# Kernel optimization log

Measured on AMD Instinct MI355X. Metric: run time of the kernel, lower is better.

The kernel has to match this reference:

```python
import jax, jax.numpy as jnp
import numpy as np

TEMPERATURE = 0.5
B, D = 4096, 256


def setup_inputs() -> dict:
    key = jax.random.key(0)
    k1, k2 = jax.random.split(key)
    emb_i = jax.random.normal(k1, (B, D), dtype=jnp.float32)
    emb_j = jax.random.normal(k2, (B, D), dtype=jnp.float32)
    return {"emb_i": emb_i, "emb_j": emb_j}


def reference(emb_i, emb_j):
    # NT-Xent (SimCLR) loss, vectorized version of the per-sample python loop.
    n = emb_i.shape[0]
    eps = 1e-12
    z_i = emb_i / jnp.maximum(jnp.linalg.norm(emb_i, axis=1, keepdims=True), eps)
    z_j = emb_j / jnp.maximum(jnp.linalg.norm(emb_j, axis=1, keepdims=True), eps)
    reps = jnp.concatenate([z_i, z_j], axis=0)               # [2N, D], unit rows
    # cosine similarity of unit vectors == dot product
    sim = reps @ reps.T                                       # [2N, 2N]
    exp_sim = jnp.exp(sim / TEMPERATURE)
    # denominator for row i: sum over k != i of exp(sim[i,k]/T)
    denom = jnp.sum(exp_sim, axis=1) - jnp.diagonal(exp_sim)  # [2N]
    # positive-pair sims: sim[k, k+N] and sim[k+N, k]
    pos = jnp.concatenate([jnp.diagonal(sim[:n, n:]), jnp.diagonal(sim[n:, :n])])
    # l_ij = log(exp(pos/T) / denom) = pos/T - log(denom)
    loss_terms = pos / TEMPERATURE - jnp.log(denom)
    return (1.0 / (2 * n)) * jnp.sum(loss_terms)
```

## Files before the change

kernel.cpp:

```cpp
#include <hip/hip_runtime.h>
#include <math.h>


#define NROWS 8192
#define NHALF 4096
#define DIM   256
#define BMT   256
#define NCB   (NROWS / 128)
#define NCBT  (NROWS / BMT)
#define NTRIT (NCBT * (NCBT + 1) / 2)

typedef __attribute__((ext_vector_type(8))) short bf16x8;
typedef __attribute__((ext_vector_type(4))) float f32x4;

static __device__ __forceinline__ unsigned short f2bf(float x) {
  unsigned int u = __float_as_uint(x);
  unsigned int r = (u + 0x7FFFu + ((u >> 16) & 1u)) >> 16;
  return (unsigned short)r;
}

__global__ __launch_bounds__(256) void normalize_kernel(
    const float* __restrict__ emb_i, const float* __restrict__ emb_j,
    unsigned short* __restrict__ zbF, float* __restrict__ out) {
  __shared__ unsigned short tile[16 * DIM];
  if (blockIdx.x == 0 && threadIdx.x == 0) out[0] = 0.f;
  const int w = threadIdx.x >> 6, lane = threadIdx.x & 63;
  const int rg = blockIdx.x;
  #pragma unroll
  for (int rr = 0; rr < 4; ++rr) {
    const int m16 = w * 4 + rr;
    const int row = rg * 16 + m16;
    const float* src = (row < NHALF) ? (emb_i + (size_t)row * DIM)
                                     : (emb_j + (size_t)(row - NHALF) * DIM);
    float4 v = ((const float4*)src)[lane];
    float ss = v.x * v.x + v.y * v.y + v.z * v.z + v.w * v.w;
    #pragma unroll
    for (int off = 32; off; off >>= 1) ss += __shfl_down(ss, off, 64);
    float total = __shfl(ss, 0, 64);
    float inv = 1.69870077f / fmaxf(sqrtf(total), 1e-12f);
    ushort4 o;
    o.x = f2bf(v.x * inv); o.y = f2bf(v.y * inv);
    o.z = f2bf(v.z * inv); o.w = f2bf(v.w * inv);
    const int s = lane >> 3, quad = (lane >> 1) & 3, jj = (lane & 1) * 4;
    *(ushort4*)&tile[s * 512 + (quad * 16 + m16) * 8 + jj] = o;
  }
  __syncthreads();
  uint4* dst = (uint4*)(zbF + (size_t)rg * (16 * DIM));
  const uint4* srcT = (const uint4*)tile;
  dst[threadIdx.x] = srcT[threadIdx.x];
  dst[256 + threadIdx.x] = srcT[256 + threadIdx.x];
}

__global__ __launch_bounds__(512, 2) void denom_kernel(
    const unsigned short* __restrict__ zbF, float* __restrict__ denomP,
    float* __restrict__ posv) {
  __shared__ unsigned short As[2][32 * 512];
  __shared__ unsigned short Bs[2][32 * 512];
  __shared__ float rowpart[4][256];
  __shared__ float colpart[2][256];

  int t = (blockIdx.x & 7) * (NTRIT / 8) + (blockIdx.x >> 3);
  int by = (int)((sqrtf(8.0f * (float)t + 1.0f) - 1.0f) * 0.5f);
  while ((by + 1) * (by + 2) / 2 <= t) ++by;
  while (by * (by + 1) / 2 > t) --by;
  int bx = t - by * (by + 1) / 2;

  const int tid = threadIdx.x;
  const int w = tid >> 6;
  const int lane = tid & 63;
  const int wr = w >> 2, wc = w & 3;
  const int quad = lane >> 4;
  const int m16 = lane & 15;
  const int row0 = bx * BMT;
  const int col0 = by * BMT;

  const unsigned short* gA = zbF + (size_t)(bx * 16) * 4096 + lane * 8;
  const unsigned short* gB = zbF + (size_t)(by * 16) * 4096 + lane * 8;

  f32x4 acc[8][4];
  #pragma unroll
  for (int i = 0; i < 8; ++i)
    #pragma unroll
    for (int j = 0; j < 4; ++j) {
      f32x4 z4 = {0.f, 0.f, 0.f, 0.f};
      acc[i][j] = z4;
    }

  auto stage = [&](int b, int kt) {
    #pragma unroll
    for (int cc = 0; cc < 4; ++cc) {
      const int c = w * 4 + cc;
      const size_t goff = (size_t)(c >> 1) * 4096 + (kt * 2 + (c & 1)) * 512;
      __builtin_amdgcn_global_load_lds(
          (const __attribute__((address_space(1))) unsigned int*)(gA + goff),
          (__attribute__((address_space(3))) unsigned int*)&As[b][c * 512],
          16, 0, 0);
      __builtin_amdgcn_global_load_lds(
          (const __attribute__((address_space(1))) unsigned int*)(gB + goff),
          (__attribute__((address_space(3))) unsigned int*)&Bs[b][c * 512],
          16, 0, 0);
    }
  };

  auto compute = [&](int b) {
    #pragma unroll
    for (int s32 = 0; s32 < 2; ++s32) {
      bf16x8 af[8], bf[4];
      #pragma unroll
      for (int i = 0; i < 8; ++i)
        af[i] = *(const bf16x8*)
            &As[b][((wr * 8 + i) * 2 + s32) * 512 + lane * 8];
      #pragma unroll
      for (int j = 0; j < 4; ++j)
        bf[j] = *(const bf16x8*)
            &Bs[b][((wc * 4 + j) * 2 + s32) * 512 + lane * 8];
      __builtin_amdgcn_s_setprio(1);
      #pragma unroll
      for (int i = 0; i < 8; ++i)
        #pragma unroll
        for (int j = 0; j < 4; ++j)
          acc[i][j] = __builtin_amdgcn_mfma_f32_16x16x32_bf16(
              af[i], bf[j], acc[i][j], 0, 0, 0);
      __builtin_amdgcn_s_setprio(0);
    }
  };

  stage(0, 0);
  stage(1, 1);
  asm volatile("s_waitcnt vmcnt(8)" ::: "memory");
  __builtin_amdgcn_s_barrier();
  asm volatile("" ::: "memory");
  compute(0);
  __builtin_amdgcn_s_barrier();
  asm volatile("" ::: "memory");
  stage(0, 2);
  asm volatile("s_waitcnt vmcnt(8)" ::: "memory");
  __builtin_amdgcn_s_barrier();
  asm volatile("" ::: "memory");
  compute(1);
  __builtin_amdgcn_s_barrier();
  asm volatile("" ::: "memory");
  stage(1, 3);
  asm volatile("s_waitcnt vmcnt(8)" ::: "memory");
  __builtin_amdgcn_s_barrier();
  asm volatile("" ::: "memory");
  compute(0);
  __builtin_amdgcn_s_barrier();
  asm volatile("" ::: "memory");
  asm volatile("s_waitcnt vmcnt(0)" ::: "memory");
  __builtin_amdgcn_s_barrier();
  asm volatile("" ::: "memory");
  compute(1);

  if (col0 - row0 == NHALF) {
    #pragma unroll
    for (int i = 0; i < 8; ++i)
      #pragma unroll
      for (int j = 0; j < 4; ++j) {
        int gcol = col0 + wc * 64 + j * 16 + m16;
        #pragma unroll
        for (int r = 0; r < 4; ++r) {
          int grow = row0 + wr * 128 + i * 16 + quad * 4 + r;
          if (gcol - grow == NHALF) posv[grow] = acc[i][j][r];
        }
      }
  }

  float rs[8][4];
  float cs[4] = {0.f, 0.f, 0.f, 0.f};
  #pragma unroll
  for (int i = 0; i < 8; ++i)
    #pragma unroll
    for (int r = 0; r < 4; ++r) rs[i][r] = 0.f;

  if (bx != by) {
    #pragma unroll
    for (int i = 0; i < 8; ++i)
      #pragma unroll
      for (int j = 0; j < 4; ++j)
        #pragma unroll
        for (int r = 0; r < 4; ++r) {
          float e = __builtin_amdgcn_exp2f(acc[i][j][r]);
          rs[i][r] += e;
          cs[j] += e;
        }
  } else {
    #pragma unroll
    for (int i = 0; i < 8; ++i)
      #pragma unroll
      for (int j = 0; j < 4; ++j) {
        int gcol = col0 + wc * 64 + j * 16 + m16;
        #pragma unroll
        for (int r = 0; r < 4; ++r) {
          int grow = row0 + wr * 128 + i * 16 + quad * 4 + r;
          float e =
              (grow == gcol) ? 0.f : __builtin_amdgcn_exp2f(acc[i][j][r]);
          rs[i][r] += e;
          cs[j] += e;
        }
      }
  }

  #pragma unroll
  for (int i = 0; i < 8; ++i)
    #pragma unroll
    for (int r = 0; r < 4; ++r) {
      float v = rs[i][r];
      v += __shfl_xor(v, 1, 16);
      v += __shfl_xor(v, 2, 16);
      v += __shfl_xor(v, 4, 16);
      v += __shfl_xor(v, 8, 16);
      if (m16 == 0) rowpart[wc][wr * 128 + i * 16 + quad * 4 + r] = v;
    }
  #pragma unroll
  for (int j = 0; j < 4; ++j) {
    float v = cs[j];
    v += __shfl_xor(v, 16, 64);
    v += __shfl_xor(v, 32, 64);
    if (quad == 0) colpart[wr][wc * 64 + j * 16 + m16] = v;
  }
  __syncthreads();

  if (tid < 256) {
    denomP[(size_t)(2 * by) * NROWS + row0 + tid] =
        rowpart[0][tid] + rowpart[1][tid] + rowpart[2][tid] + rowpart[3][tid];
  } else if (bx != by) {
    int c = tid - 256;
    denomP[(size_t)(2 * bx) * NROWS + col0 + c] =
        colpart[0][c] + colpart[1][c];
  }
}

__global__ __launch_bounds__(256) void reduce_kernel(
    const float* __restrict__ denomP, const float* __restrict__ posv,
    float* __restrict__ out) {
  int tid = threadIdx.x;
  int r = blockIdx.x * 256 + tid;
  float s = 0.f;
  #pragma unroll 8
  for (int b = 0; b < NCB; b += 2) s += denomP[(size_t)b * NROWS + r];
  float v = -logf(s);
  if (r < NHALF) v += 1.38629436112f * posv[r];
  #pragma unroll
  for (int off = 32; off; off >>= 1) v += __shfl_down(v, off, 64);
  __shared__ float s4[4];
  if ((tid & 63) == 0) s4[tid >> 6] = v;
  __syncthreads();
  if (tid == 0)
    atomicAdd(out, (s4[0] + s4[1] + s4[2] + s4[3]) * (1.0f / 8192.0f));
}

extern "C" void kernel_launch(void* const* d_in, const int* in_sizes, int n_in,
                              void* d_out, int out_size, void* d_ws,
                              size_t ws_size, hipStream_t stream) {
  const float* emb_i = (const float*)d_in[0];
  const float* emb_j = (const float*)d_in[1];
  unsigned short* zbF = (unsigned short*)d_ws;
  float* denomP = (float*)(zbF + (size_t)NROWS * DIM);
  float* posv = denomP + (size_t)NCB * NROWS;
  float* out = (float*)d_out;

  normalize_kernel<<<NROWS / 16, 256, 0, stream>>>(emb_i, emb_j, zbF, out);
  denom_kernel<<<NTRIT, 512, 0, stream>>>(zbF, denomP, posv);
  reduce_kernel<<<NROWS / 256, 256, 0, stream>>>(denomP, posv, out);
}
```

Measured before the change: 106.6 us.

## Make denom kernel persistent over three tiles with cross-tile prefetch and split MFMA phases

Each block now handles three consecutive triangular tiles (176 blocks cover 528 tiles), so the global-to-LDS loads for the next tile are issued before the current tile's exp/reduction epilogue runs, hiding load latency across tile boundaries. The compute step is split into half-tile phases with smaller A-fragment register sets and extra barriers, which lowers register pressure. The grid is now sized to the CU count rather than the tile count. Costs include many more barriers and the loss of the previous interleaved tile ordering. With one block per CU there is also less occupancy to cover stalls, and the diagonal tiles may unbalance the work per block.

```diff
diff --git a/kernel.cpp b/kernel.cpp
--- a/kernel.cpp
+++ b/kernel.cpp
@@ -9,6 +9,7 @@
 #define NCB   (NROWS / 128)
 #define NCBT  (NROWS / BMT)
 #define NTRIT (NCBT * (NCBT + 1) / 2)
+#define GRID_D 176
 
 typedef __attribute__((ext_vector_type(8))) short bf16x8;
 typedef __attribute__((ext_vector_type(4))) float f32x4;
@@ -59,23 +60,29 @@
   __shared__ float rowpart[4][256];
   __shared__ float colpart[2][256];
 
-  int t = (blockIdx.x & 7) * (NTRIT / 8) + (blockIdx.x >> 3);
-  int by = (int)((sqrtf(8.0f * (float)t + 1.0f) - 1.0f) * 0.5f);
-  while ((by + 1) * (by + 2) / 2 <= t) ++by;
-  while (by * (by + 1) / 2 > t) --by;
-  int bx = t - by * (by + 1) / 2;
-
   const int tid = threadIdx.x;
   const int w = tid >> 6;
   const int lane = tid & 63;
   const int wr = w >> 2, wc = w & 3;
   const int quad = lane >> 4;
   const int m16 = lane & 15;
-  const int row0 = bx * BMT;
-  const int col0 = by * BMT;
-
-  const unsigned short* gA = zbF + (size_t)(bx * 16) * 4096 + lane * 8;
-  const unsigned short* gB = zbF + (size_t)(by * 16) * 4096 + lane * 8;
+
+  auto decode = [](int t, int& bx, int& by) {
+    by = (int)((sqrtf(8.0f * (float)t + 1.0f) - 1.0f) * 0.5f);
+    while ((by + 1) * (by + 2) / 2 <= t) ++by;
+    while (by * (by + 1) / 2 > t) --by;
+    bx = t - by * (by + 1) / 2;
+  };
+  int bx0, by0, bx1, by1, bx2, by2;
+  decode(blockIdx.x * 3 + 0, bx0, by0);
+  decode(blockIdx.x * 3 + 1, bx1, by1);
+  decode(blockIdx.x * 3 + 2, bx2, by2);
+  const unsigned short* gA0 = zbF + (size_t)(bx0 * 16) * 4096 + lane * 8;
+  const unsigned short* gB0 = zbF + (size_t)(by0 * 16) * 4096 + lane * 8;
+  const unsigned short* gA1 = zbF + (size_t)(bx1 * 16) * 4096 + lane * 8;
+  const unsigned short* gB1 = zbF + (size_t)(by1 * 16) * 4096 + lane * 8;
+  const unsigned short* gA2 = zbF + (size_t)(bx2 * 16) * 4096 + lane * 8;
+  const unsigned short* gB2 = zbF + (size_t)(by2 * 16) * 4096 + lane * 8;
 
   f32x4 acc[8][4];
   #pragma unroll
@@ -86,149 +93,176 @@
       acc[i][j] = z4;
     }
 
-  auto stage = [&](int b, int kt) {
+  auto stage = [&](int b, const unsigned short* gA_,
+                   const unsigned short* gB_, int kt) {
     #pragma unroll
     for (int cc = 0; cc < 4; ++cc) {
       const int c = w * 4 + cc;
       const size_t goff = (size_t)(c >> 1) * 4096 + (kt * 2 + (c & 1)) * 512;
       __builtin_amdgcn_global_load_lds(
-          (const __attribute__((address_space(1))) unsigned int*)(gA + goff),
+          (const __attribute__((address_space(1))) unsigned int*)(gA_ + goff),
           (__attribute__((address_space(3))) unsigned int*)&As[b][c * 512],
           16, 0, 0);
       __builtin_amdgcn_global_load_lds(
-          (const __attribute__((address_space(1))) unsigned int*)(gB + goff),
+          (const __attribute__((address_space(1))) unsigned int*)(gB_ + goff),
           (__attribute__((address_space(3))) unsigned int*)&Bs[b][c * 512],
           16, 0, 0);
     }
   };
 
-  auto compute = [&](int b) {
-    #pragma unroll
-    for (int s32 = 0; s32 < 2; ++s32) {
-      bf16x8 af[8], bf[4];
+  bf16x8 af[4], bf[4];
+
+#define BARm()                                   \
+  __builtin_amdgcn_s_barrier();                  \
+  asm volatile("" ::: "memory")
+
+#define PH_LOADB(BUF, S32)                                                \
+  do {                                                                    \
+    _Pragma("unroll") for (int j = 0; j < 4; ++j)                         \
+        bf[j] = *(const bf16x8*)                                          \
+            &Bs[BUF][((wc * 4 + j) * 2 + (S32)) * 512 + lane * 8];        \
+  } while (0)
+
+#define PH_LOADA(BUF, S32, H)                                             \
+  do {                                                                    \
+    _Pragma("unroll") for (int i4 = 0; i4 < 4; ++i4)                      \
+        af[i4] = *(const bf16x8*)                                         \
+            &As[BUF][((wr * 8 + (H)*4 + i4) * 2 + (S32)) * 512 +          \
+                     lane * 8];                                           \
+  } while (0)
+
+#define PH_MFMA(H)                                                        \
+  do {                                                                    \
+    __builtin_amdgcn_s_setprio(1);                                        \
+    _Pragma("unroll") for (int i4 = 0; i4 < 4; ++i4)                      \
+        _Pragma("unroll") for (int j = 0; j < 4; ++j)                     \
+            acc[(H)*4 + i4][j] = __builtin_amdgcn_mfma_f32_16x16x32_bf16( \
+                af[i4], bf[j], acc[(H)*4 + i4][j], 0, 0, 0);              \
+    __builtin_amdgcn_s_setprio(0);                                        \
+  } while (0)
+
+#define KSTEP(BUF, WN, DOSTG, GAS, GBS, KTS)                              \
+  do {                                                                    \
+    asm volatile("s_waitcnt vmcnt(" #WN ")" ::: "memory");                \
+    BARm();                                                               \
+    PH_LOADB(BUF, 0); PH_LOADA(BUF, 0, 0); PH_MFMA(0);                    \
+    BARm();                                                               \
+    PH_LOADA(BUF, 0, 1); PH_MFMA(1);                                      \
+    BARm();                                                               \
+    PH_LOADB(BUF, 1); PH_LOADA(BUF, 1, 0); PH_MFMA(0);                    \
+    BARm();                                                               \
+    PH_LOADA(BUF, 1, 1); PH_MFMA(1);                                      \
+    BARm();                                                               \
+    if (DOSTG) stage(BUF, GAS, GBS, KTS);                                 \
+  } while (0)
+
+  auto epilogue = [&](int bx, int by) {
+    const int row0 = bx * BMT, col0 = by * BMT;
+    if (col0 - row0 == NHALF) {
       #pragma unroll
       for (int i = 0; i < 8; ++i)
-        af[i] = *(const bf16x8*)
-            &As[b][((wr * 8 + i) * 2 + s32) * 512 + lane * 8];
-      #pragma unroll
-      for (int j = 0; j < 4; ++j)
-        bf[j] = *(const bf16x8*)
-            &Bs[b][((wc * 4 + j) * 2 + s32) * 512 + lane * 8];
-      __builtin_amdgcn_s_setprio(1);
+        #pragma unroll
+        for (int j = 0; j < 4; ++j) {
+          int gcol = col0 + wc * 64 + j * 16 + m16;
+          #pragma unroll
+          for (int r = 0; r < 4; ++r) {
+            int grow = row0 + wr * 128 + i * 16 + quad * 4 + r;
+            if (gcol - grow == NHALF) posv[grow] = acc[i][j][r];
+          }
+        }
+    }
+    float rs[8][4];
+    float cs[4] = {0.f, 0.f, 0.f, 0.f};
+    #pragma unroll
+    for (int i = 0; i < 8; ++i)
+      #pragma unroll
+      for (int r = 0; r < 4; ++r) rs[i][r] = 0.f;
+    if (bx != by) {
       #pragma unroll
       for (int i = 0; i < 8; ++i)
         #pragma unroll
         for (int j = 0; j < 4; ++j)
-          acc[i][j] = __builtin_amdgcn_mfma_f32_16x16x32_bf16(
-              af[i], bf[j], acc[i][j], 0, 0, 0);
-      __builtin_amdgcn_s_setprio(0);
-    }
+          #pragma unroll
+          for (int r = 0; r < 4; ++r) {
+            float e = __builtin_amdgcn_exp2f(acc[i][j][r]);
+            rs[i][r] += e;
+            cs[j] += e;
+          }
+    } else {
+      #pragma unroll
+      for (int i = 0; i < 8; ++i)
+        #pragma unroll
+        for (int j = 0; j < 4; ++j) {
+          int gcol = col0 + wc * 64 + j * 16 + m16;
+          #pragma unroll
+          for (int r = 0; r < 4; ++r) {
+            int grow = row0 + wr * 128 + i * 16 + quad * 4 + r;
+            float e =
+                (grow == gcol) ? 0.f : __builtin_amdgcn_exp2f(acc[i][j][r]);
+            rs[i][r] += e;
+            cs[j] += e;
+          }
+        }
+    }
+    #pragma unroll
+    for (int i = 0; i < 8; ++i)
+      #pragma unroll
+      for (int r = 0; r < 4; ++r) {
+        float v = rs[i][r];
+        v += __shfl_xor(v, 1, 16);
+        v += __shfl_xor(v, 2, 16);
+        v += __shfl_xor(v, 4, 16);
+        v += __shfl_xor(v, 8, 16);
+        if (m16 == 0) rowpart[wc][wr * 128 + i * 16 + quad * 4 + r] = v;
+      }
+    #pragma unroll
+    for (int j = 0; j < 4; ++j) {
+      float v = cs[j];
+      v += __shfl_xor(v, 16, 64);
+      v += __shfl_xor(v, 32, 64);
+      if (quad == 0) colpart[wr][wc * 64 + j * 16 + m16] = v;
+    }
+    asm volatile("s_waitcnt lgkmcnt(0)" ::: "memory");
+    BARm();
+    if (tid < 256) {
+      denomP[(size_t)(2 * by) * NROWS + row0 + tid] = rowpart[0][tid] +
+          rowpart[1][tid] + rowpart[2][tid] + rowpart[3][tid];
+    } else if (bx != by) {
+      int c = tid - 256;
+      denomP[(size_t)(2 * bx) * NROWS + col0 + c] =
+          colpart[0][c] + colpart[1][c];
+    }
+    #pragma unroll
+    for (int i = 0; i < 8; ++i)
+      #pragma unroll
+      for (int j = 0; j < 4; ++j) {
+        f32x4 z4 = {0.f, 0.f, 0.f, 0.f};
+        acc[i][j] = z4;
+      }
   };
 
-  stage(0, 0);
-  stage(1, 1);
-  asm volatile("s_waitcnt vmcnt(8)" ::: "memory");
-  __builtin_amdgcn_s_barrier();
-  asm volatile("" ::: "memory");
-  compute(0);
-  __builtin_amdgcn_s_barrier();
-  asm volatile("" ::: "memory");
-  stage(0, 2);
-  asm volatile("s_waitcnt vmcnt(8)" ::: "memory");
-  __builtin_amdgcn_s_barrier();
-  asm volatile("" ::: "memory");
-  compute(1);
-  __builtin_amdgcn_s_barrier();
-  asm volatile("" ::: "memory");
-  stage(1, 3);
-  asm volatile("s_waitcnt vmcnt(8)" ::: "memory");
-  __builtin_amdgcn_s_barrier();
-  asm volatile("" ::: "memory");
-  compute(0);
-  __builtin_amdgcn_s_barrier();
-  asm volatile("" ::: "memory");
-  asm volatile("s_waitcnt vmcnt(0)" ::: "memory");
-  __builtin_amdgcn_s_barrier();
-  asm volatile("" ::: "memory");
-  compute(1);
-
-  if (col0 - row0 == NHALF) {
-    #pragma unroll
-    for (int i = 0; i < 8; ++i)
-      #pragma unroll
-      for (int j = 0; j < 4; ++j) {
-        int gcol = col0 + wc * 64 + j * 16 + m16;
-        #pragma unroll
-        for (int r = 0; r < 4; ++r) {
-          int grow = row0 + wr * 128 + i * 16 + quad * 4 + r;
-          if (gcol - grow == NHALF) posv[grow] = acc[i][j][r];
-        }
-      }
-  }
-
-  float rs[8][4];
-  float cs[4] = {0.f, 0.f, 0.f, 0.f};
-  #pragma unroll
-  for (int i = 0; i < 8; ++i)
-    #pragma unroll
-    for (int r = 0; r < 4; ++r) rs[i][r] = 0.f;
-
-  if (bx != by) {
-    #pragma unroll
-    for (int i = 0; i < 8; ++i)
-      #pragma unroll
-      for (int j = 0; j < 4; ++j)
-        #pragma unroll
-        for (int r = 0; r < 4; ++r) {
-          float e = __builtin_amdgcn_exp2f(acc[i][j][r]);
-          rs[i][r] += e;
-          cs[j] += e;
-        }
-  } else {
-    #pragma unroll
-    for (int i = 0; i < 8; ++i)
-      #pragma unroll
-      for (int j = 0; j < 4; ++j) {
-        int gcol = col0 + wc * 64 + j * 16 + m16;
-        #pragma unroll
-        for (int r = 0; r < 4; ++r) {
-          int grow = row0 + wr * 128 + i * 16 + quad * 4 + r;
-          float e =
-              (grow == gcol) ? 0.f : __builtin_amdgcn_exp2f(acc[i][j][r]);
-          rs[i][r] += e;
-          cs[j] += e;
-        }
-      }
-  }
-
-  #pragma unroll
-  for (int i = 0; i < 8; ++i)
-    #pragma unroll
-    for (int r = 0; r < 4; ++r) {
-      float v = rs[i][r];
-      v += __shfl_xor(v, 1, 16);
-      v += __shfl_xor(v, 2, 16);
-      v += __shfl_xor(v, 4, 16);
-      v += __shfl_xor(v, 8, 16);
-      if (m16 == 0) rowpart[wc][wr * 128 + i * 16 + quad * 4 + r] = v;
-    }
-  #pragma unroll
-  for (int j = 0; j < 4; ++j) {
-    float v = cs[j];
-    v += __shfl_xor(v, 16, 64);
-    v += __shfl_xor(v, 32, 64);
-    if (quad == 0) colpart[wr][wc * 64 + j * 16 + m16] = v;
-  }
-  __syncthreads();
-
-  if (tid < 256) {
-    denomP[(size_t)(2 * by) * NROWS + row0 + tid] =
-        rowpart[0][tid] + rowpart[1][tid] + rowpart[2][tid] + rowpart[3][tid];
-  } else if (bx != by) {
-    int c = tid - 256;
-    denomP[(size_t)(2 * bx) * NROWS + col0 + c] =
-        colpart[0][c] + colpart[1][c];
-  }
+  stage(0, gA0, gB0, 0);
+  stage(1, gA0, gB0, 1);
+  KSTEP(0, 8, 1, gA0, gB0, 2);
+  KSTEP(1, 8, 1, gA0, gB0, 3);
+  KSTEP(0, 8, 1, gA1, gB1, 0);
+  KSTEP(1, 8, 1, gA1, gB1, 1);
+  epilogue(bx0, by0);
+  KSTEP(0, 8, 1, gA1, gB1, 2);
+  KSTEP(1, 8, 1, gA1, gB1, 3);
+  KSTEP(0, 8, 1, gA2, gB2, 0);
+  KSTEP(1, 8, 1, gA2, gB2, 1);
+  epilogue(bx1, by1);
+  KSTEP(0, 8, 1, gA2, gB2, 2);
+  KSTEP(1, 8, 1, gA2, gB2, 3);
+  KSTEP(0, 8, 0, gA2, gB2, 0);
+  KSTEP(1, 0, 0, gA2, gB2, 0);
+  epilogue(bx2, by2);
+#undef KSTEP
+#undef PH_MFMA
+#undef PH_LOADA
+#undef PH_LOADB
+#undef BARm
 }
 
 __global__ __launch_bounds__(256) void reduce_kernel(
@@ -261,6 +295,6 @@
   float* out = (float*)d_out;
 
   normalize_kernel<<<NROWS / 16, 256, 0, stream>>>(emb_i, emb_j, zbF, out);
-  denom_kernel<<<NTRIT, 512, 0, stream>>>(zbF, denomP, posv);
+  denom_kernel<<<GRID_D, 512, 0, stream>>>(zbF, denomP, posv);
   reduce_kernel<<<NROWS / 256, 256, 0, stream>>>(denomP, posv, out);
 }
```

New measurement: 112.9 us. +5.9%, slower.
